# Kernel optimization log

Hardware: AMD Instinct MI355X
Metric: run time of the kernel (lower is better)

## Reference

```python
import jax, jax.numpy as jnp
import numpy as np
from jax import lax

O, C, K = 256, 64, 3          # out_channels, in_channels, kernel size
M = 9                          # ALSH augmentation terms (m)
EXTRA = M // (K * K)           # channels Q appends to the input (=1)
D = C + EXTRA                  # d = in_channels + m/(k*k)
T = 8192                       # table_size
R = 4.0                        # hash bucket width hash.r
STRIDE, PAD = 1, 1


def _P(kernels):
    # ALSH preprocessing: flatten each kernel and append powers of its squared norm
    flat = kernels.reshape(O, -1)                        # [O, C*K*K]
    n2 = jnp.sum(flat * flat, axis=1, keepdims=True)     # [O, 1]
    pows = jnp.concatenate([n2 ** (i + 1) for i in range(M)], axis=1)  # [O, M]
    return jnp.concatenate([flat, pows], axis=1)         # [O, C*K*K + M]


def _hash(a, b, x):
    # x: [n, C*K*K + M];  floor((a . x + b) / r)
    return jnp.floor((x @ a + b) / R)


def setup_inputs():
    key = jax.random.key(0)
    k1, k2, k3, k4 = jax.random.split(key, 4)
    inp = jax.random.normal(k1, (16, C, 256, 256), jnp.float32)
    kernels = jax.random.normal(k2, (O, C, K, K), jnp.float32) * 0.04
    a = jax.random.normal(k3, (D * K * K,), jnp.float32)
    b = jax.random.uniform(k4, (1,), jnp.float32) * R
    return {"input": inp, "kernels": kernels, "a": a, "b": b}


def reference(input, kernels, a, b):
    N, _, H, W = input.shape
    # ---- init_table: hash every kernel into a bucket (vectorized scatter) ----
    hk = _hash(a, b[0], _P(kernels))                     # [O]
    idx = jnp.abs(jnp.fmod(hk, T)).astype(jnp.int32)     # torch: fmod_ then abs_
    onehot = jax.nn.one_hot(idx, T, dtype=jnp.int32)     # [O, T]
    excl = jnp.cumsum(onehot, axis=0) - onehot           # slot within bucket (insertion order)
    pos = jnp.take_along_axis(excl, idx[:, None], axis=1)[:, 0]
    table = jnp.zeros((T, 2 * O), jnp.int32).at[idx, pos].set(
        jnp.arange(O, dtype=jnp.int32))
    row_len = jnp.sum(onehot, axis=0)                    # [T] bucket sizes
    # ---- vote: hash every conv patch via a 1-output-channel convolution ----
    inp_q = jnp.concatenate(
        [input, jnp.full((N, EXTRA, H, W), 0.5, input.dtype)], axis=1)  # Q(input)
    kern = a.reshape(1, D, K, K)
    dotted = lax.conv_general_dilated(inp_q, kern, (STRIDE, STRIDE),
                                      [(PAD, PAD), (PAD, PAD)])
    votes = jnp.floor((dotted.reshape(-1) + b[0]) / R)   # [N*H'*W']
    vidx = jnp.abs(jnp.fmod(votes, T)).astype(jnp.int32)
    count = jax.ops.segment_sum(jnp.ones_like(votes), vidx, num_segments=T)
    index = jnp.argmax(count)
    # ---- gather active set (fixed-size padded gather, sorted rows) ----
    L = row_len[index]
    slot = jnp.arange(2 * O)
    rows = jnp.where(slot < L, table[index], O)          # sentinel O sorts to the end
    rows = jnp.sort(rows)
    valid = (slot < L).astype(kernels.dtype)
    active = kernels[jnp.clip(rows, 0, O - 1)] * valid[:, None, None, None]
    return active, count, index.astype(jnp.int32)
```

## Files before the change

kernel.cpp:

```cpp
#include <hip/hip_runtime.h>

#define O_CH   256
#define C_CH   64
#define FLATK  576
#define M_TERMS 9
#define AL     585
#define TSZ    8192
#define RADIUS 4.0f
#define NB     16
#define HH     256
#define WW     256

#define WS_KIDX 0
#define WS_HIST 256
#define WS_BEST (256 + TSZ)
#define WS_ROWS (256 + TSZ + 1)

__global__ __launch_bounds__(256) void k_init(const float* __restrict__ kernels,
                                              const float* __restrict__ a,
                                              const float* __restrict__ b,
                                              int* __restrict__ ws) {
    if (blockIdx.x < 64) {
        const int wv = threadIdx.x >> 6, lane = threadIdx.x & 63;
        const int o = blockIdx.x * 4 + wv;
        const float* wp = kernels + o * FLATK;
        float dot = 0.f, n2 = 0.f;
        #pragma unroll
        for (int j0 = 0; j0 < FLATK; j0 += 64) {
            float x = wp[j0 + lane];
            dot += x * a[j0 + lane];
            n2  += x * x;
        }
        #pragma unroll
        for (int off = 32; off > 0; off >>= 1) {
            dot += __shfl_xor(dot, off);
            n2  += __shfl_xor(n2, off);
        }
        if (lane == 0) {
            float p = n2, d = dot;
            for (int i = 0; i < M_TERMS; ++i) { d += p * a[FLATK + i]; p *= n2; }
            float hk = floorf((d + b[0]) / RADIUS);
            ws[WS_KIDX + o] = (int)fabsf(fmodf(hk, (float)TSZ));
        }
    } else {
        int t = (blockIdx.x - 64) * 256 + threadIdx.x;
        ws[WS_HIST + t] = 0;
    }
}

#define TILE_H 8
__global__ __launch_bounds__(256) void k_vote(const float* __restrict__ input,
                                              const float* __restrict__ a,
                                              const float* __restrict__ b,
                                              int* __restrict__ ws) {
    __shared__ int   hist_s[TSZ];
    __shared__ float a_s[AL];
    const int tid = threadIdx.x;

    for (int i = tid; i < TSZ; i += 256) hist_s[i] = 0;
    for (int i = tid; i < AL; i += 256) a_s[i] = a[i];
    __syncthreads();

    const float bv = b[0];
    const int by = blockIdx.x & 31;
    const int n  = blockIdx.x >> 5;
    const int y0 = by * TILE_H;
    const int lane = tid & 63;
    const int yg = tid >> 6;
    const int x4 = lane * 4;
    const int ybase = y0 + yg * 2;

    float acc[2][4] = {{0.f,0.f,0.f,0.f},{0.f,0.f,0.f,0.f}};
    const float* imgbase = input + (size_t)n * C_CH * HH * WW;

    float4 vbuf[2][4];
    #pragma unroll
    for (int r = 0; r < 4; ++r) {
        int gy = ybase - 1 + r;
        vbuf[0][r] = (gy >= 0 && gy < HH)
                   ? *(const float4*)(imgbase + gy * WW + x4)
                   : make_float4(0.f, 0.f, 0.f, 0.f);
    }

    #pragma unroll 2
    for (int c = 0; c < C_CH; ++c) {
        const int cur = c & 1, nxt = cur ^ 1;
        if (c + 1 < C_CH) {
            const float* src = imgbase + (size_t)(c + 1) * (HH * WW);
            #pragma unroll
            for (int r = 0; r < 4; ++r) {
                int gy = ybase - 1 + r;
                vbuf[nxt][r] = (gy >= 0 && gy < HH)
                             ? *(const float4*)(src + gy * WW + x4)
                             : make_float4(0.f, 0.f, 0.f, 0.f);
            }
        }
        float win[4][6];
        #pragma unroll
        for (int r = 0; r < 4; ++r) {
            float4 v = vbuf[cur][r];
            float lv = __shfl_up(v.w, 1);   if (lane == 0)  lv = 0.f;
            float rv = __shfl_down(v.x, 1); if (lane == 63) rv = 0.f;
            win[r][0] = lv; win[r][1] = v.x; win[r][2] = v.y;
            win[r][3] = v.z; win[r][4] = v.w; win[r][5] = rv;
        }
        const float* ac = a_s + c * 9;
        #pragma unroll
        for (int rr = 0; rr < 2; ++rr)
            #pragma unroll
            for (int ky = 0; ky < 3; ++ky)
                #pragma unroll
                for (int p = 0; p < 4; ++p)
                    #pragma unroll
                    for (int kx = 0; kx < 3; ++kx)
                        acc[rr][p] += win[rr + ky][p + kx] * ac[ky * 3 + kx];
    }

    #pragma unroll
    for (int rr = 0; rr < 2; ++rr) {
        int gy = ybase + rr;
        #pragma unroll
        for (int p = 0; p < 4; ++p) {
            int gx = x4 + p;
            float cs = 0.f;
            #pragma unroll
            for (int ky = 0; ky < 3; ++ky) {
                int yy = gy + ky - 1;
                if (yy < 0 || yy >= HH) continue;
                #pragma unroll
                for (int kx = 0; kx < 3; ++kx) {
                    int xx = gx + kx - 1;
                    if (xx < 0 || xx >= WW) continue;
                    cs += a_s[FLATK + ky * 3 + kx];
                }
            }
            float t = acc[rr][p] + 0.5f * cs;
            float v = floorf((t + bv) / RADIUS);
            int vi = (int)fabsf(fmodf(v, (float)TSZ));
            atomicAdd(&hist_s[vi], 1);
        }
    }

    __syncthreads();
    int* hist_g = ws + WS_HIST;
    for (int i = tid; i < TSZ; i += 256) {
        int v = hist_s[i];
        if (v) atomicAdd(&hist_g[i], v);
    }
}

__global__ __launch_bounds__(256) void k_finalize(int* __restrict__ ws,
                                                  float* __restrict__ out) {
    __shared__ int sv[256], si[256];
    __shared__ int wsum[4];
    const int tid = threadIdx.x;
    const int* hist = ws + WS_HIST;

    int best = -1, bidx = 0;
    for (int t = tid; t < TSZ; t += 256) {
        int v = hist[t];
        if (v > best) { best = v; bidx = t; }
    }
    sv[tid] = best; si[tid] = bidx;
    __syncthreads();
    for (int s = 128; s > 0; s >>= 1) {
        if (tid < s) {
            if (sv[tid + s] > sv[tid] ||
                (sv[tid + s] == sv[tid] && si[tid + s] < si[tid])) {
                sv[tid] = sv[tid + s]; si[tid] = si[tid + s];
            }
        }
        __syncthreads();
    }
    const int bestIdx = si[0];

    float* count_out = out + 512 * FLATK;
    for (int t = tid; t < TSZ; t += 256) count_out[t] = (float)hist[t];
    if (tid == 0) {
        out[512 * FLATK + TSZ] = (float)bestIdx;
        ws[WS_BEST] = bestIdx;
    }

    int* rows = ws + WS_ROWS;
    for (int i = tid; i < 2 * O_CH; i += 256) rows[i] = -1;
    const int o = tid;
    const int match = (ws[WS_KIDX + o] == bestIdx) ? 1 : 0;
    unsigned long long m = __ballot(match);
    const int lane = tid & 63, wv = tid >> 6;
    if (lane == 0) wsum[wv] = __popcll(m);
    __syncthreads();
    int prefix = 0;
    for (int i = 0; i < wv; ++i) prefix += wsum[i];
    int before = __popcll(m & ((1ull << lane) - 1ull));
    if (match) rows[prefix + before] = o;
}

__global__ void k_gather(const float* __restrict__ kernels,
                         const int* __restrict__ ws,
                         float* __restrict__ out) {
    int gid = blockIdx.x * blockDim.x + threadIdx.x;
    if (gid >= 2 * O_CH * FLATK) return;
    int s = gid / FLATK;
    int j = gid - s * FLATK;
    int r = ws[WS_ROWS + s];
    out[gid] = (r >= 0) ? kernels[r * FLATK + j] : 0.0f;
}

extern "C" void kernel_launch(void* const* d_in, const int* in_sizes, int n_in,
                              void* d_out, int out_size, void* d_ws, size_t ws_size,
                              hipStream_t stream) {
    const float* input   = (const float*)d_in[0];
    const float* kernels = (const float*)d_in[1];
    const float* a       = (const float*)d_in[2];
    const float* b       = (const float*)d_in[3];
    float* out = (float*)d_out;
    int*   ws  = (int*)d_ws;

    k_init<<<96, 256, 0, stream>>>(kernels, a, b, ws);
    k_vote<<<NB * (HH / TILE_H), 256, 0, stream>>>(input, a, b, ws);
    k_finalize<<<1, 256, 0, stream>>>(ws, out);
    k_gather<<<(2 * O_CH * FLATK + 255) / 256, 256, 0, stream>>>(kernels, ws, out);
}
```

Before: 409.7 us.

## Split conv channel reduction across blocks and reduce partials in separate vote kernel

The per-patch hash convolution is split into four channel groups, each computed by its own block, which writes partial sums to workspace scratch. A second kernel sums the four partials, adds the augmentation term, and builds the bucket histogram. This raises the block count and removes the large shared histogram from the conv kernel, so more waves can hide memory latency. In exchange it adds a scratch write/read pass and an extra launch, and the float summation order changes.

Result: no change. 406.6 us (-0.8%).

```diff
diff --git a/kernel.cpp b/kernel.cpp
--- a/kernel.cpp
+++ b/kernel.cpp
@@ -10,11 +10,14 @@
 #define NB     16
 #define HH     256
 #define WW     256
+#define CG     4
+#define CPG    (C_CH / CG)
 
 #define WS_KIDX 0
 #define WS_HIST 256
 #define WS_BEST (256 + TSZ)
 #define WS_ROWS (256 + TSZ + 1)
+#define WS_SCRATCH_F 32768
 
 __global__ __launch_bounds__(256) void k_init(const float* __restrict__ kernels,
                                               const float* __restrict__ a,
@@ -49,16 +52,88 @@
 }
 
 #define TILE_H 8
-__global__ __launch_bounds__(256) void k_vote(const float* __restrict__ input,
-                                              const float* __restrict__ a,
-                                              const float* __restrict__ b,
-                                              int* __restrict__ ws) {
-    __shared__ int   hist_s[TSZ];
-    __shared__ float a_s[AL];
+__global__ __launch_bounds__(256) void k_conv_part(const float* __restrict__ input,
+                                                   const float* __restrict__ a,
+                                                   float* __restrict__ ps) {
+    __shared__ float a_s[C_CH * 9];
     const int tid = threadIdx.x;
-
+    for (int i = tid; i < C_CH * 9; i += 256) a_s[i] = a[i];
+    __syncthreads();
+
+    const int g  = blockIdx.x & (CG - 1);
+    const int t2 = blockIdx.x >> 2;
+    const int by = t2 & 31;
+    const int n  = t2 >> 5;
+    const int y0 = by * TILE_H;
+    const int lane = tid & 63;
+    const int yg = tid >> 6;
+    const int x4 = lane * 4;
+    const int ybase = y0 + yg * 2;
+    const int c0 = g * CPG;
+
+    float acc[2][4] = {{0.f,0.f,0.f,0.f},{0.f,0.f,0.f,0.f}};
+    const float* imgbase = input + (size_t)n * C_CH * HH * WW;
+
+    float4 vbuf[2][4];
+    #pragma unroll
+    for (int r = 0; r < 4; ++r) {
+        int gy = ybase - 1 + r;
+        vbuf[0][r] = (gy >= 0 && gy < HH)
+                   ? *(const float4*)(imgbase + (size_t)c0 * (HH * WW) + gy * WW + x4)
+                   : make_float4(0.f, 0.f, 0.f, 0.f);
+    }
+
+    #pragma unroll 2
+    for (int cc = 0; cc < CPG; ++cc) {
+        const int c = c0 + cc;
+        const int cur = cc & 1, nxt = cur ^ 1;
+        if (cc + 1 < CPG) {
+            const float* src = imgbase + (size_t)(c + 1) * (HH * WW);
+            #pragma unroll
+            for (int r = 0; r < 4; ++r) {
+                int gy = ybase - 1 + r;
+                vbuf[nxt][r] = (gy >= 0 && gy < HH)
+                             ? *(const float4*)(src + gy * WW + x4)
+                             : make_float4(0.f, 0.f, 0.f, 0.f);
+            }
+        }
+        float win[4][6];
+        #pragma unroll
+        for (int r = 0; r < 4; ++r) {
+            float4 v = vbuf[cur][r];
+            float lv = __shfl_up(v.w, 1);   if (lane == 0)  lv = 0.f;
+            float rv = __shfl_down(v.x, 1); if (lane == 63) rv = 0.f;
+            win[r][0] = lv; win[r][1] = v.x; win[r][2] = v.y;
+            win[r][3] = v.z; win[r][4] = v.w; win[r][5] = rv;
+        }
+        const float* ac = a_s + c * 9;
+        #pragma unroll
+        for (int rr = 0; rr < 2; ++rr)
+            #pragma unroll
+            for (int ky = 0; ky < 3; ++ky)
+                #pragma unroll
+                for (int p = 0; p < 4; ++p)
+                    #pragma unroll
+                    for (int kx = 0; kx < 3; ++kx)
+                        acc[rr][p] += win[rr + ky][p + kx] * ac[ky * 3 + kx];
+    }
+
+    float* dst = ps + ((size_t)(g * NB + n) * HH) * WW;
+    #pragma unroll
+    for (int rr = 0; rr < 2; ++rr)
+        *(float4*)(dst + (ybase + rr) * WW + x4) =
+            make_float4(acc[rr][0], acc[rr][1], acc[rr][2], acc[rr][3]);
+}
+
+__global__ __launch_bounds__(256) void k_vote2(const float* __restrict__ ps,
+                                               const float* __restrict__ a,
+                                               const float* __restrict__ b,
+                                               int* __restrict__ ws) {
+    __shared__ int hist_s[TSZ];
+    __shared__ float aq_s[9];
+    const int tid = threadIdx.x;
     for (int i = tid; i < TSZ; i += 256) hist_s[i] = 0;
-    for (int i = tid; i < AL; i += 256) a_s[i] = a[i];
+    if (tid < 9) aq_s[tid] = a[FLATK + tid];
     __syncthreads();
 
     const float bv = b[0];
@@ -70,55 +145,16 @@
     const int x4 = lane * 4;
     const int ybase = y0 + yg * 2;
 
-    float acc[2][4] = {{0.f,0.f,0.f,0.f},{0.f,0.f,0.f,0.f}};
-    const float* imgbase = input + (size_t)n * C_CH * HH * WW;
-
-    float4 vbuf[2][4];
-    #pragma unroll
-    for (int r = 0; r < 4; ++r) {
-        int gy = ybase - 1 + r;
-        vbuf[0][r] = (gy >= 0 && gy < HH)
-                   ? *(const float4*)(imgbase + gy * WW + x4)
-                   : make_float4(0.f, 0.f, 0.f, 0.f);
-    }
-
-    #pragma unroll 2
-    for (int c = 0; c < C_CH; ++c) {
-        const int cur = c & 1, nxt = cur ^ 1;
-        if (c + 1 < C_CH) {
-            const float* src = imgbase + (size_t)(c + 1) * (HH * WW);
-            #pragma unroll
-            for (int r = 0; r < 4; ++r) {
-                int gy = ybase - 1 + r;
-                vbuf[nxt][r] = (gy >= 0 && gy < HH)
-                             ? *(const float4*)(src + gy * WW + x4)
-                             : make_float4(0.f, 0.f, 0.f, 0.f);
-            }
-        }
-        float win[4][6];
-        #pragma unroll
-        for (int r = 0; r < 4; ++r) {
-            float4 v = vbuf[cur][r];
-            float lv = __shfl_up(v.w, 1);   if (lane == 0)  lv = 0.f;
-            float rv = __shfl_down(v.x, 1); if (lane == 63) rv = 0.f;
-            win[r][0] = lv; win[r][1] = v.x; win[r][2] = v.y;
-            win[r][3] = v.z; win[r][4] = v.w; win[r][5] = rv;
-        }
-        const float* ac = a_s + c * 9;
-        #pragma unroll
-        for (int rr = 0; rr < 2; ++rr)
-            #pragma unroll
-            for (int ky = 0; ky < 3; ++ky)
-                #pragma unroll
-                for (int p = 0; p < 4; ++p)
-                    #pragma unroll
-                    for (int kx = 0; kx < 3; ++kx)
-                        acc[rr][p] += win[rr + ky][p + kx] * ac[ky * 3 + kx];
-    }
-
     #pragma unroll
     for (int rr = 0; rr < 2; ++rr) {
-        int gy = ybase + rr;
+        const int gy = ybase + rr;
+        float4 s = make_float4(0.f, 0.f, 0.f, 0.f);
+        #pragma unroll
+        for (int g = 0; g < CG; ++g) {
+            float4 v = *(const float4*)(ps + ((size_t)(g * NB + n) * HH + gy) * WW + x4);
+            s.x += v.x; s.y += v.y; s.z += v.z; s.w += v.w;
+        }
+        float accv[4] = {s.x, s.y, s.z, s.w};
         #pragma unroll
         for (int p = 0; p < 4; ++p) {
             int gx = x4 + p;
@@ -131,10 +167,10 @@
                 for (int kx = 0; kx < 3; ++kx) {
                     int xx = gx + kx - 1;
                     if (xx < 0 || xx >= WW) continue;
-                    cs += a_s[FLATK + ky * 3 + kx];
+                    cs += aq_s[ky * 3 + kx];
                 }
             }
-            float t = acc[rr][p] + 0.5f * cs;
+            float t = accv[p] + 0.5f * cs;
             float v = floorf((t + bv) / RADIUS);
             int vi = (int)fabsf(fmodf(v, (float)TSZ));
             atomicAdd(&hist_s[vi], 1);
@@ -215,9 +251,11 @@
     const float* b       = (const float*)d_in[3];
     float* out = (float*)d_out;
     int*   ws  = (int*)d_ws;
+    float* ps  = (float*)d_ws + WS_SCRATCH_F;
 
     k_init<<<96, 256, 0, stream>>>(kernels, a, b, ws);
-    k_vote<<<NB * (HH / TILE_H), 256, 0, stream>>>(input, a, b, ws);
+    k_conv_part<<<NB * (HH / TILE_H) * CG, 256, 0, stream>>>(input, a, ps);
+    k_vote2<<<NB * (HH / TILE_H), 256, 0, stream>>>(ps, a, b, ws);
     k_finalize<<<1, 256, 0, stream>>>(ws, out);
     k_gather<<<(2 * O_CH * FLATK + 255) / 256, 256, 0, stream>>>(kernels, ws, out);
 }
```
